# Optimization experiments

Hardware: AMD Instinct MI355X
Metric: run time of the kernel (lower is better)

The kernel has to match this reference:

```python
import jax, jax.numpy as jnp
import numpy as np

EPS = 1e-8  # torch F.cosine_similarity eps


def _l2norm(x):
    # x / max(||x||, eps), matching torch cosine_similarity's clamped denominator
    n = jnp.sqrt(jnp.sum(x * x, axis=-1, keepdims=True))
    return x / jnp.maximum(n, EPS)


def setup_inputs() -> dict:
    key = jax.random.key(0)
    k1, k2, k3 = jax.random.split(key, 3)
    B, S, C, D = 16, 512, 16, 512
    return {
        "output": jax.random.normal(k1, (B, C), dtype=jnp.float32),
        "target_text_feats": jax.random.normal(k2, (B, S, C, D), dtype=jnp.float32),
        "vis_feats": jax.random.normal(k3, (B, S, D), dtype=jnp.float32),
    }


def reference(output, target_text_feats, vis_feats):
    B, S, C, D = target_text_feats.shape
    vn = _l2norm(vis_feats)              # (B, S, D)
    tn = _l2norm(target_text_feats)      # (B, S, C, D)
    # sim[b,p,v,t] = cos(vis[b,v], text[b,t,p]); replaces the per-prompt python loop
    sim = jnp.einsum('bvd,btpd->bpvt', vn, tn)  # (B, C, S, S)
    diag = jnp.diagonal(sim, axis1=-2, axis2=-1)      # (B, C, S): sim[b,p,i,i]
    lse_row = jax.nn.logsumexp(sim, axis=-1)          # CE over text axis (logits_per_image)
    lse_col = jax.nn.logsumexp(sim, axis=-2)          # CE over vis axis  (logits_per_text)
    # per-sample clip loss, averaged over the v axis -> (B, C)
    clip_loss = jnp.mean(0.5 * (lse_row + lse_col) - diag, axis=-1)
    clip_loss = jax.lax.stop_gradient(clip_loss)      # computed under torch.no_grad()

    loss = jnp.mean(jnp.square(output - clip_loss))

    gt_labels = jnp.argmin(clip_loss, axis=-1)        # (B,)
    preds = jnp.argmin(output, axis=-1)               # (B,)
    acc = jnp.mean((preds == gt_labels).astype(jnp.float32)) * 100.0
    prompt_id_preds = jnp.broadcast_to(preds[:, None, None], (B, S, 1))
    return loss, acc, prompt_id_preds
```

## Files before the change

kernel.cpp:

```cpp
#include <hip/hip_runtime.h>

#define EPSN 1e-8f

typedef _Float16 half8 __attribute__((ext_vector_type(8)));
typedef float floatx4 __attribute__((ext_vector_type(4)));

__global__ __launch_bounds__(256) void k_vinv(const float* __restrict__ vis,
                                              float* __restrict__ vinv) {
    int row  = blockIdx.x * 4 + (threadIdx.x >> 6);
    int lane = threadIdx.x & 63;
    const float4* src = reinterpret_cast<const float4*>(vis + (size_t)row * 512);
    float4 a = src[lane];
    float4 b = src[lane + 64];
    float s = a.x*a.x + a.y*a.y + a.z*a.z + a.w*a.w
            + b.x*b.x + b.y*b.y + b.z*b.z + b.w*b.w;
    #pragma unroll
    for (int off = 1; off < 64; off <<= 1) s += __shfl_xor(s, off);
    if (lane == 0) vinv[row] = 1.0f / fmaxf(sqrtf(s), EPSN);
}

#define LDA 40
#define LDB 40

__global__ __launch_bounds__(256, 2) void k_main(
    const float* __restrict__ vis, const float* __restrict__ text,
    const float* __restrict__ vinv,
    float* __restrict__ g_rowsum, float* __restrict__ g_colsum,
    float* __restrict__ g_dsum)
{
    __shared__ _Float16 Ash[256 * LDA];
    __shared__ _Float16 Bsh[128 * LDB];
    __shared__ float tn2[128];
    __shared__ float colS[128];

    const int blk  = blockIdx.x;
    const int vh   = blk & 1;
    const int tb   = (blk >> 1) & 3;
    const int bp   = blk >> 3;
    const int p    = bp & 15;
    const int b    = bp >> 4;
    const int tid  = threadIdx.x;
    const int lane = tid & 63;
    const int wave = tid >> 6;
    const int v0   = vh * 256;
    const int t0   = tb * 128;
    const int m15  = lane & 15;
    const int g4   = lane >> 4;

    if (tid < 128) colS[tid] = 0.f;

    floatx4 acc[4][8];
    floatx4 zf = {0.f, 0.f, 0.f, 0.f};
    #pragma unroll
    for (int mb = 0; mb < 4; ++mb)
        #pragma unroll
        for (int nb = 0; nb < 8; ++nb) acc[mb][nb] = zf;

    const float* visB = vis + (size_t)b * 512 * 512 + (size_t)v0 * 512;
    const int arow = tid >> 2;
    const int ako  = (tid & 3) * 8;
    const int brow0 = tid >> 2;
    const int brow1 = 64 + (tid >> 2);
    const int bko  = (tid & 3) * 8;
    const float* textRow0 =
        text + ((size_t)((b * 512 + t0 + brow0) * 16 + p)) * 512;
    const float* textRow1 =
        text + ((size_t)((b * 512 + t0 + brow1) * 16 + p)) * 512;

    float sq0 = 0.f, sq1 = 0.f;

    for (int kc = 0; kc < 16; ++kc) {
        const int k0 = kc * 32;
        #pragma unroll
        for (int c = 0; c < 4; ++c) {
            int row = c * 64 + arow;
            const float4* s4 =
                reinterpret_cast<const float4*>(visB + (size_t)row * 512 + k0 + ako);
            float4 f0 = s4[0], f1 = s4[1];
            half8 h = { (_Float16)f0.x, (_Float16)f0.y, (_Float16)f0.z, (_Float16)f0.w,
                        (_Float16)f1.x, (_Float16)f1.y, (_Float16)f1.z, (_Float16)f1.w };
            *reinterpret_cast<half8*>(&Ash[row * LDA + ako]) = h;
        }
        {
            const float4* s4 = reinterpret_cast<const float4*>(textRow0 + k0 + bko);
            float4 f0 = s4[0], f1 = s4[1];
            sq0 += f0.x*f0.x + f0.y*f0.y + f0.z*f0.z + f0.w*f0.w
                 + f1.x*f1.x + f1.y*f1.y + f1.z*f1.z + f1.w*f1.w;
            half8 h = { (_Float16)f0.x, (_Float16)f0.y, (_Float16)f0.z, (_Float16)f0.w,
                        (_Float16)f1.x, (_Float16)f1.y, (_Float16)f1.z, (_Float16)f1.w };
            *reinterpret_cast<half8*>(&Bsh[brow0 * LDB + bko]) = h;
        }
        {
            const float4* s4 = reinterpret_cast<const float4*>(textRow1 + k0 + bko);
            float4 f0 = s4[0], f1 = s4[1];
            sq1 += f0.x*f0.x + f0.y*f0.y + f0.z*f0.z + f0.w*f0.w
                 + f1.x*f1.x + f1.y*f1.y + f1.z*f1.z + f1.w*f1.w;
            half8 h = { (_Float16)f0.x, (_Float16)f0.y, (_Float16)f0.z, (_Float16)f0.w,
                        (_Float16)f1.x, (_Float16)f1.y, (_Float16)f1.z, (_Float16)f1.w };
            *reinterpret_cast<half8*>(&Bsh[brow1 * LDB + bko]) = h;
        }
        __syncthreads();
        half8 af[4];
        #pragma unroll
        for (int mb = 0; mb < 4; ++mb)
            af[mb] = *reinterpret_cast<const half8*>(
                &Ash[(wave * 64 + mb * 16 + m15) * LDA + g4 * 8]);
        #pragma unroll
        for (int nb = 0; nb < 8; ++nb) {
            half8 bf = *reinterpret_cast<const half8*>(
                &Bsh[(nb * 16 + m15) * LDB + g4 * 8]);
            #pragma unroll
            for (int mb = 0; mb < 4; ++mb)
                acc[mb][nb] = __builtin_amdgcn_mfma_f32_16x16x32_f16(
                    af[mb], bf, acc[mb][nb], 0, 0, 0);
        }
        __syncthreads();
    }

    sq0 += __shfl_xor(sq0, 1); sq0 += __shfl_xor(sq0, 2);
    sq1 += __shfl_xor(sq1, 1); sq1 += __shfl_xor(sq1, 2);
    if ((tid & 3) == 0) {
        tn2[brow0] = 1.0f / fmaxf(sqrtf(sq0), EPSN);
        tn2[brow1] = 1.0f / fmaxf(sqrtf(sq1), EPSN);
    }
    __syncthreads();

    float tinvc[8];
    #pragma unroll
    for (int nb = 0; nb < 8; ++nb) tinvc[nb] = tn2[nb * 16 + m15];

    float colpart[8];
    #pragma unroll
    for (int nb = 0; nb < 8; ++nb) colpart[nb] = 0.f;
    float dsum = 0.f;

    #pragma unroll
    for (int mb = 0; mb < 4; ++mb) {
        #pragma unroll
        for (int r = 0; r < 4; ++r) {
            int vglob = v0 + wave * 64 + mb * 16 + g4 * 4 + r;
            float vi  = vinv[b * 512 + vglob];
            float rp  = 0.f;
            #pragma unroll
            for (int nb = 0; nb < 8; ++nb) {
                float sim  = acc[mb][nb][r] * vi * tinvc[nb];
                int tglob  = t0 + nb * 16 + m15;
                if (vglob == tglob) dsum += sim;
                float e = __expf(sim);
                rp += e;
                colpart[nb] += e;
            }
            rp += __shfl_xor(rp, 1);
            rp += __shfl_xor(rp, 2);
            rp += __shfl_xor(rp, 4);
            rp += __shfl_xor(rp, 8);
            if (m15 == 0)
                atomicAdd(&g_rowsum[(size_t)bp * 512 + vglob], rp);
        }
    }
    #pragma unroll
    for (int nb = 0; nb < 8; ++nb) {
        float cp = colpart[nb];
        cp += __shfl_xor(cp, 16);
        cp += __shfl_xor(cp, 32);
        if (lane < 16) atomicAdd(&colS[nb * 16 + lane], cp);
    }
    #pragma unroll
    for (int off = 1; off < 64; off <<= 1) dsum += __shfl_xor(dsum, off);
    if (lane == 0) atomicAdd(&g_dsum[bp], dsum);
    __syncthreads();
    if (tid < 128)
        atomicAdd(&g_colsum[(size_t)bp * 512 + t0 + tid], colS[tid]);
}

__global__ __launch_bounds__(256) void k_clip(
    const float* __restrict__ g_rowsum, const float* __restrict__ g_colsum,
    const float* __restrict__ g_dsum, float* __restrict__ clip)
{
    __shared__ float red[4];
    int bp = blockIdx.x, tid = threadIdx.x;
    int lane = tid & 63, wave = tid >> 6;
    float s = 0.f;
    #pragma unroll
    for (int c = 0; c < 2; ++c) {
        int i = c * 256 + tid;
        s += 0.5f * (logf(g_rowsum[(size_t)bp * 512 + i]) +
                     logf(g_colsum[(size_t)bp * 512 + i]));
    }
    #pragma unroll
    for (int off = 1; off < 64; off <<= 1) s += __shfl_xor(s, off);
    if (lane == 0) red[wave] = s;
    __syncthreads();
    if (tid == 0)
        clip[bp] = (red[0] + red[1] + red[2] + red[3] - g_dsum[bp]) * (1.0f / 512.0f);
}

__global__ __launch_bounds__(256) void k_final(
    const float* __restrict__ clip, const float* __restrict__ output,
    float* __restrict__ out)
{
    __shared__ float cl[256], ou[256], red[4];
    __shared__ int preds[16];
    int tid = threadIdx.x, lane = tid & 63, wave = tid >> 6;
    cl[tid] = clip[tid];
    ou[tid] = output[tid];
    __syncthreads();
    float d = ou[tid] - cl[tid];
    float s = d * d;
    #pragma unroll
    for (int off = 1; off < 64; off <<= 1) s += __shfl_xor(s, off);
    if (lane == 0) red[wave] = s;
    if (tid < 16) {
        float m = ou[tid * 16]; int a = 0;
        for (int q = 1; q < 16; ++q)
            if (ou[tid * 16 + q] < m) { m = ou[tid * 16 + q]; a = q; }
        preds[tid] = a;
    }
    __syncthreads();
    if (tid == 0) {
        int cnt = 0;
        for (int bb = 0; bb < 16; ++bb) {
            float m = cl[bb * 16]; int a = 0;
            for (int q = 1; q < 16; ++q)
                if (cl[bb * 16 + q] < m) { m = cl[bb * 16 + q]; a = q; }
            cnt += (preds[bb] == a);
        }
        out[0] = (red[0] + red[1] + red[2] + red[3]) * (1.0f / 256.0f);
        out[1] = (float)cnt * (100.0f / 16.0f);
    }
    __syncthreads();
    for (int j = tid; j < 16 * 512; j += 256)
        out[2 + j] = (float)preds[j >> 9];
}

extern "C" void kernel_launch(void* const* d_in, const int* in_sizes, int n_in,
                              void* d_out, int out_size, void* d_ws, size_t ws_size,
                              hipStream_t stream)
{
    const float* output = (const float*)d_in[0];
    const float* text   = (const float*)d_in[1];
    const float* vis    = (const float*)d_in[2];

    float* g_rowsum = (float*)d_ws;
    float* g_colsum = g_rowsum + 256 * 512;
    float* g_dsum   = g_colsum + 256 * 512;
    float* clip     = g_dsum + 256;
    float* vinv     = clip + 256;
    hipMemsetAsync(d_ws, 0, (size_t)(2 * 256 * 512 + 256) * sizeof(float), stream);

    k_vinv <<<2048, 256, 0, stream>>>(vis, vinv);
    k_main <<<2048, 256, 0, stream>>>(vis, text, vinv, g_rowsum, g_colsum, g_dsum);
    k_clip <<<256, 256, 0, stream>>>(g_rowsum, g_colsum, g_dsum, clip);
    k_final<<<1, 256, 0, stream>>>(clip, output, (float*)d_out);
}
```

Measured before the change: 482.6 us.

## Prefetch next K-chunk into registers, fuse vis norm into main kernel, use packed cvt

Loads for the next K chunk of vis and text are issued into registers before the current chunk's shared-memory store completes, so global latency overlaps with MFMA work. The vis row norms are accumulated inside k_main from the same loaded data, which removes the separate k_vinv launch and its extra pass over vis. Float-to-half conversion switches to the packed round-toward-zero instruction. In exchange, register pressure rises from the 16 extra float4 prefetch registers, the last iteration issues a wasted wrap-around load, and rounding changes slightly from round-to-nearest to round-toward-zero.

Result: no change. 476.1 us (-1.4%).

```diff
diff --git a/kernel.cpp b/kernel.cpp
--- a/kernel.cpp
+++ b/kernel.cpp
@@ -3,34 +3,21 @@
 #define EPSN 1e-8f
 
 typedef _Float16 half8 __attribute__((ext_vector_type(8)));
+typedef __fp16 fp16x2 __attribute__((ext_vector_type(2)));
 typedef float floatx4 __attribute__((ext_vector_type(4)));
-
-__global__ __launch_bounds__(256) void k_vinv(const float* __restrict__ vis,
-                                              float* __restrict__ vinv) {
-    int row  = blockIdx.x * 4 + (threadIdx.x >> 6);
-    int lane = threadIdx.x & 63;
-    const float4* src = reinterpret_cast<const float4*>(vis + (size_t)row * 512);
-    float4 a = src[lane];
-    float4 b = src[lane + 64];
-    float s = a.x*a.x + a.y*a.y + a.z*a.z + a.w*a.w
-            + b.x*b.x + b.y*b.y + b.z*b.z + b.w*b.w;
-    #pragma unroll
-    for (int off = 1; off < 64; off <<= 1) s += __shfl_xor(s, off);
-    if (lane == 0) vinv[row] = 1.0f / fmaxf(sqrtf(s), EPSN);
-}
 
 #define LDA 40
 #define LDB 40
 
 __global__ __launch_bounds__(256, 2) void k_main(
     const float* __restrict__ vis, const float* __restrict__ text,
-    const float* __restrict__ vinv,
     float* __restrict__ g_rowsum, float* __restrict__ g_colsum,
     float* __restrict__ g_dsum)
 {
     __shared__ _Float16 Ash[256 * LDA];
     __shared__ _Float16 Bsh[128 * LDB];
     __shared__ float tn2[128];
+    __shared__ float vinvS[256];
     __shared__ float colS[128];
 
     const int blk  = blockIdx.x;
@@ -59,45 +46,67 @@
     const float* visB = vis + (size_t)b * 512 * 512 + (size_t)v0 * 512;
     const int arow = tid >> 2;
     const int ako  = (tid & 3) * 8;
-    const int brow0 = tid >> 2;
-    const int brow1 = 64 + (tid >> 2);
-    const int bko  = (tid & 3) * 8;
-    const float* textRow0 =
-        text + ((size_t)((b * 512 + t0 + brow0) * 16 + p)) * 512;
-    const float* textRow1 =
-        text + ((size_t)((b * 512 + t0 + brow1) * 16 + p)) * 512;
-
+    const float* aBase = visB + (size_t)arow * 512 + ako;
+    const float* tPtr0 =
+        text + ((size_t)((b * 512 + t0 + (tid >> 2)) * 16 + p)) * 512 + (tid & 3) * 8;
+    const float* tPtr1 = tPtr0 + (size_t)64 * 16 * 512;
+
+    float vsq[4] = {0.f, 0.f, 0.f, 0.f};
     float sq0 = 0.f, sq1 = 0.f;
 
+    float4 abuf[4][2];
+    #pragma unroll
+    for (int c = 0; c < 4; ++c) {
+        abuf[c][0] = *reinterpret_cast<const float4*>(aBase + c * 64 * 512);
+        abuf[c][1] = *reinterpret_cast<const float4*>(aBase + c * 64 * 512 + 4);
+    }
+    float4 bbuf[2][2];
+    bbuf[0][0] = *reinterpret_cast<const float4*>(tPtr0);
+    bbuf[0][1] = *reinterpret_cast<const float4*>(tPtr0 + 4);
+    bbuf[1][0] = *reinterpret_cast<const float4*>(tPtr1);
+    bbuf[1][1] = *reinterpret_cast<const float4*>(tPtr1 + 4);
+
     for (int kc = 0; kc < 16; ++kc) {
-        const int k0 = kc * 32;
+        const int kn = ((kc + 1) & 15) * 32;
         #pragma unroll
         for (int c = 0; c < 4; ++c) {
-            int row = c * 64 + arow;
-            const float4* s4 =
-                reinterpret_cast<const float4*>(visB + (size_t)row * 512 + k0 + ako);
-            float4 f0 = s4[0], f1 = s4[1];
-            half8 h = { (_Float16)f0.x, (_Float16)f0.y, (_Float16)f0.z, (_Float16)f0.w,
-                        (_Float16)f1.x, (_Float16)f1.y, (_Float16)f1.z, (_Float16)f1.w };
-            *reinterpret_cast<half8*>(&Ash[row * LDA + ako]) = h;
+            float4 f0 = abuf[c][0], f1 = abuf[c][1];
+            vsq[c] += f0.x*f0.x + f0.y*f0.y + f0.z*f0.z + f0.w*f0.w
+                    + f1.x*f1.x + f1.y*f1.y + f1.z*f1.z + f1.w*f1.w;
+            union { half8 v; fp16x2 p[4]; } u;
+            u.p[0] = __builtin_amdgcn_cvt_pkrtz(f0.x, f0.y);
+            u.p[1] = __builtin_amdgcn_cvt_pkrtz(f0.z, f0.w);
+            u.p[2] = __builtin_amdgcn_cvt_pkrtz(f1.x, f1.y);
+            u.p[3] = __builtin_amdgcn_cvt_pkrtz(f1.z, f1.w);
+            *reinterpret_cast<half8*>(&Ash[(c * 64 + arow) * LDA + ako]) = u.v;
+            abuf[c][0] = *reinterpret_cast<const float4*>(aBase + c * 64 * 512 + kn);
+            abuf[c][1] = *reinterpret_cast<const float4*>(aBase + c * 64 * 512 + kn + 4);
         }
         {
-            const float4* s4 = reinterpret_cast<const float4*>(textRow0 + k0 + bko);
-            float4 f0 = s4[0], f1 = s4[1];
+            float4 f0 = bbuf[0][0], f1 = bbuf[0][1];
             sq0 += f0.x*f0.x + f0.y*f0.y + f0.z*f0.z + f0.w*f0.w
                  + f1.x*f1.x + f1.y*f1.y + f1.z*f1.z + f1.w*f1.w;
-            half8 h = { (_Float16)f0.x, (_Float16)f0.y, (_Float16)f0.z, (_Float16)f0.w,
-                        (_Float16)f1.x, (_Float16)f1.y, (_Float16)f1.z, (_Float16)f1.w };
-            *reinterpret_cast<half8*>(&Bsh[brow0 * LDB + bko]) = h;
+            union { half8 v; fp16x2 p[4]; } u;
+            u.p[0] = __builtin_amdgcn_cvt_pkrtz(f0.x, f0.y);
+            u.p[1] = __builtin_amdgcn_cvt_pkrtz(f0.z, f0.w);
+            u.p[2] = __builtin_amdgcn_cvt_pkrtz(f1.x, f1.y);
+            u.p[3] = __builtin_amdgcn_cvt_pkrtz(f1.z, f1.w);
+            *reinterpret_cast<half8*>(&Bsh[(tid >> 2) * LDB + (tid & 3) * 8]) = u.v;
+            bbuf[0][0] = *reinterpret_cast<const float4*>(tPtr0 + kn);
+            bbuf[0][1] = *reinterpret_cast<const float4*>(tPtr0 + kn + 4);
         }
         {
-            const float4* s4 = reinterpret_cast<const float4*>(textRow1 + k0 + bko);
-            float4 f0 = s4[0], f1 = s4[1];
+            float4 f0 = bbuf[1][0], f1 = bbuf[1][1];
             sq1 += f0.x*f0.x + f0.y*f0.y + f0.z*f0.z + f0.w*f0.w
                  + f1.x*f1.x + f1.y*f1.y + f1.z*f1.z + f1.w*f1.w;
-            half8 h = { (_Float16)f0.x, (_Float16)f0.y, (_Float16)f0.z, (_Float16)f0.w,
-                        (_Float16)f1.x, (_Float16)f1.y, (_Float16)f1.z, (_Float16)f1.w };
-            *reinterpret_cast<half8*>(&Bsh[brow1 * LDB + bko]) = h;
+            union { half8 v; fp16x2 p[4]; } u;
+            u.p[0] = __builtin_amdgcn_cvt_pkrtz(f0.x, f0.y);
+            u.p[1] = __builtin_amdgcn_cvt_pkrtz(f0.z, f0.w);
+            u.p[2] = __builtin_amdgcn_cvt_pkrtz(f1.x, f1.y);
+            u.p[3] = __builtin_amdgcn_cvt_pkrtz(f1.z, f1.w);
+            *reinterpret_cast<half8*>(&Bsh[(64 + (tid >> 2)) * LDB + (tid & 3) * 8]) = u.v;
+            bbuf[1][0] = *reinterpret_cast<const float4*>(tPtr1 + kn);
+            bbuf[1][1] = *reinterpret_cast<const float4*>(tPtr1 + kn + 4);
         }
         __syncthreads();
         half8 af[4];
@@ -117,11 +126,18 @@
         __syncthreads();
     }
 
+    #pragma unroll
+    for (int c = 0; c < 4; ++c) {
+        float s = vsq[c];
+        s += __shfl_xor(s, 1); s += __shfl_xor(s, 2);
+        if ((lane & 3) == 0)
+            vinvS[c * 64 + arow] = 1.0f / fmaxf(sqrtf(s), EPSN);
+    }
     sq0 += __shfl_xor(sq0, 1); sq0 += __shfl_xor(sq0, 2);
     sq1 += __shfl_xor(sq1, 1); sq1 += __shfl_xor(sq1, 2);
     if ((tid & 3) == 0) {
-        tn2[brow0] = 1.0f / fmaxf(sqrtf(sq0), EPSN);
-        tn2[brow1] = 1.0f / fmaxf(sqrtf(sq1), EPSN);
+        tn2[tid >> 2] = 1.0f / fmaxf(sqrtf(sq0), EPSN);
+        tn2[64 + (tid >> 2)] = 1.0f / fmaxf(sqrtf(sq1), EPSN);
     }
     __syncthreads();
 
@@ -138,8 +154,9 @@
     for (int mb = 0; mb < 4; ++mb) {
         #pragma unroll
         for (int r = 0; r < 4; ++r) {
-            int vglob = v0 + wave * 64 + mb * 16 + g4 * 4 + r;
-            float vi  = vinv[b * 512 + vglob];
+            int vloc  = wave * 64 + mb * 16 + g4 * 4 + r;
+            int vglob = v0 + vloc;
+            float vi  = vinvS[vloc];
             float rp  = 0.f;
             #pragma unroll
             for (int nb = 0; nb < 8; ++nb) {
@@ -245,11 +262,9 @@
     float* g_colsum = g_rowsum + 256 * 512;
     float* g_dsum   = g_colsum + 256 * 512;
     float* clip     = g_dsum + 256;
-    float* vinv     = clip + 256;
-    hipMemsetAsync(d_ws, 0, (size_t)(2 * 256 * 512 + 256) * sizeof(float), stream);
-
-    k_vinv <<<2048, 256, 0, stream>>>(vis, vinv);
-    k_main <<<2048, 256, 0, stream>>>(vis, text, vinv, g_rowsum, g_colsum, g_dsum);
+    (void)hipMemsetAsync(d_ws, 0, (size_t)(2 * 256 * 512 + 256) * sizeof(float), stream);
+
+    k_main <<<2048, 256, 0, stream>>>(vis, text, g_rowsum, g_colsum, g_dsum);
     k_clip <<<256, 256, 0, stream>>>(g_rowsum, g_colsum, g_dsum, clip);
     k_final<<<1, 256, 0, stream>>>(clip, output, (float*)d_out);
 }
```

## Use 128x128 tiles with 2x2 wave layout and fuse vis-norm into main kernel

Applied to the files above, without the earlier changes.

Changes the GEMM tile from 256x128 to 128x128 per block, with a 2x2 wave arrangement and 4096 blocks at occupancy hint 4. The vis row norms are now computed inside the main kernel instead of a separate k_vinv launch. Row sums are accumulated in shared memory before one global atomic per row, and fp32-to-fp16 conversion uses packed cvt_pkrtz. The smaller tile reloads the vis and text operands more often (text reads double), which may raise memory traffic on an already bandwidth-heavy kernel; pkrtz rounds toward zero rather than to nearest.

Result: slower. 494.7 us (+2.5%).

```diff
diff --git a/kernel.cpp b/kernel.cpp
--- a/kernel.cpp
+++ b/kernel.cpp
@@ -3,112 +3,110 @@
 #define EPSN 1e-8f
 
 typedef _Float16 half8 __attribute__((ext_vector_type(8)));
+typedef __fp16 fp16x2 __attribute__((ext_vector_type(2)));
 typedef float floatx4 __attribute__((ext_vector_type(4)));
 
-__global__ __launch_bounds__(256) void k_vinv(const float* __restrict__ vis,
-                                              float* __restrict__ vinv) {
-    int row  = blockIdx.x * 4 + (threadIdx.x >> 6);
-    int lane = threadIdx.x & 63;
-    const float4* src = reinterpret_cast<const float4*>(vis + (size_t)row * 512);
-    float4 a = src[lane];
-    float4 b = src[lane + 64];
-    float s = a.x*a.x + a.y*a.y + a.z*a.z + a.w*a.w
-            + b.x*b.x + b.y*b.y + b.z*b.z + b.w*b.w;
-    #pragma unroll
-    for (int off = 1; off < 64; off <<= 1) s += __shfl_xor(s, off);
-    if (lane == 0) vinv[row] = 1.0f / fmaxf(sqrtf(s), EPSN);
-}
-
 #define LDA 40
-#define LDB 40
-
-__global__ __launch_bounds__(256, 2) void k_main(
+
+__global__ __launch_bounds__(256, 4) void k_main(
     const float* __restrict__ vis, const float* __restrict__ text,
-    const float* __restrict__ vinv,
     float* __restrict__ g_rowsum, float* __restrict__ g_colsum,
     float* __restrict__ g_dsum)
 {
-    __shared__ _Float16 Ash[256 * LDA];
-    __shared__ _Float16 Bsh[128 * LDB];
+    __shared__ _Float16 Ash[128 * LDA];
+    __shared__ _Float16 Bsh[128 * LDA];
     __shared__ float tn2[128];
+    __shared__ float vinvS[128];
+    __shared__ float rowS[128];
     __shared__ float colS[128];
 
     const int blk  = blockIdx.x;
-    const int vh   = blk & 1;
-    const int tb   = (blk >> 1) & 3;
-    const int bp   = blk >> 3;
+    const int vq   = blk & 3;
+    const int tb   = (blk >> 2) & 3;
+    const int bp   = blk >> 4;
     const int p    = bp & 15;
     const int b    = bp >> 4;
     const int tid  = threadIdx.x;
     const int lane = tid & 63;
     const int wave = tid >> 6;
-    const int v0   = vh * 256;
-    const int t0   = tb * 128;
+    const int wy   = wave >> 1;
+    const int wx   = wave & 1;
     const int m15  = lane & 15;
     const int g4   = lane >> 4;
 
-    if (tid < 128) colS[tid] = 0.f;
-
-    floatx4 acc[4][8];
+    if (tid < 128) { rowS[tid] = 0.f; colS[tid] = 0.f; }
+
+    floatx4 acc[4][4];
     floatx4 zf = {0.f, 0.f, 0.f, 0.f};
     #pragma unroll
     for (int mb = 0; mb < 4; ++mb)
         #pragma unroll
-        for (int nb = 0; nb < 8; ++nb) acc[mb][nb] = zf;
-
-    const float* visB = vis + (size_t)b * 512 * 512 + (size_t)v0 * 512;
-    const int arow = tid >> 2;
-    const int ako  = (tid & 3) * 8;
-    const int brow0 = tid >> 2;
-    const int brow1 = 64 + (tid >> 2);
-    const int bko  = (tid & 3) * 8;
-    const float* textRow0 =
-        text + ((size_t)((b * 512 + t0 + brow0) * 16 + p)) * 512;
-    const float* textRow1 =
-        text + ((size_t)((b * 512 + t0 + brow1) * 16 + p)) * 512;
-
-    float sq0 = 0.f, sq1 = 0.f;
+        for (int nb = 0; nb < 4; ++nb) acc[mb][nb] = zf;
+
+    const int srow = tid >> 1;
+    const int sko  = (tid & 1) * 16;
+    const float* aPtr =
+        vis + (size_t)b * 512 * 512 + (size_t)(vq * 128 + srow) * 512 + sko;
+    const float* bPtr =
+        text + ((size_t)((b * 512 + tb * 128 + srow) * 16 + p)) * 512 + sko;
+
+    float vsq = 0.f, tsq = 0.f;
 
     for (int kc = 0; kc < 16; ++kc) {
-        const int k0 = kc * 32;
-        #pragma unroll
-        for (int c = 0; c < 4; ++c) {
-            int row = c * 64 + arow;
-            const float4* s4 =
-                reinterpret_cast<const float4*>(visB + (size_t)row * 512 + k0 + ako);
-            float4 f0 = s4[0], f1 = s4[1];
-            half8 h = { (_Float16)f0.x, (_Float16)f0.y, (_Float16)f0.z, (_Float16)f0.w,
-                        (_Float16)f1.x, (_Float16)f1.y, (_Float16)f1.z, (_Float16)f1.w };
-            *reinterpret_cast<half8*>(&Ash[row * LDA + ako]) = h;
-        }
+        float4 a0 = *reinterpret_cast<const float4*>(aPtr);
+        float4 a1 = *reinterpret_cast<const float4*>(aPtr + 4);
+        float4 a2 = *reinterpret_cast<const float4*>(aPtr + 8);
+        float4 a3 = *reinterpret_cast<const float4*>(aPtr + 12);
+        float4 b0 = *reinterpret_cast<const float4*>(bPtr);
+        float4 b1 = *reinterpret_cast<const float4*>(bPtr + 4);
+        float4 b2 = *reinterpret_cast<const float4*>(bPtr + 8);
+        float4 b3 = *reinterpret_cast<const float4*>(bPtr + 12);
+        aPtr += 32; bPtr += 32;
+
+        vsq += a0.x*a0.x + a0.y*a0.y + a0.z*a0.z + a0.w*a0.w
+             + a1.x*a1.x + a1.y*a1.y + a1.z*a1.z + a1.w*a1.w
+             + a2.x*a2.x + a2.y*a2.y + a2.z*a2.z + a2.w*a2.w
+             + a3.x*a3.x + a3.y*a3.y + a3.z*a3.z + a3.w*a3.w;
         {
-            const float4* s4 = reinterpret_cast<const float4*>(textRow0 + k0 + bko);
-            float4 f0 = s4[0], f1 = s4[1];
-            sq0 += f0.x*f0.x + f0.y*f0.y + f0.z*f0.z + f0.w*f0.w
-                 + f1.x*f1.x + f1.y*f1.y + f1.z*f1.z + f1.w*f1.w;
-            half8 h = { (_Float16)f0.x, (_Float16)f0.y, (_Float16)f0.z, (_Float16)f0.w,
-                        (_Float16)f1.x, (_Float16)f1.y, (_Float16)f1.z, (_Float16)f1.w };
-            *reinterpret_cast<half8*>(&Bsh[brow0 * LDB + bko]) = h;
-        }
+            union { half8 v; fp16x2 q[4]; } u;
+            u.q[0] = __builtin_amdgcn_cvt_pkrtz(a0.x, a0.y);
+            u.q[1] = __builtin_amdgcn_cvt_pkrtz(a0.z, a0.w);
+            u.q[2] = __builtin_amdgcn_cvt_pkrtz(a1.x, a1.y);
+            u.q[3] = __builtin_amdgcn_cvt_pkrtz(a1.z, a1.w);
+            *reinterpret_cast<half8*>(&Ash[srow * LDA + sko]) = u.v;
+            u.q[0] = __builtin_amdgcn_cvt_pkrtz(a2.x, a2.y);
+            u.q[1] = __builtin_amdgcn_cvt_pkrtz(a2.z, a2.w);
+            u.q[2] = __builtin_amdgcn_cvt_pkrtz(a3.x, a3.y);
+            u.q[3] = __builtin_amdgcn_cvt_pkrtz(a3.z, a3.w);
+            *reinterpret_cast<half8*>(&Ash[srow * LDA + sko + 8]) = u.v;
+        }
+        tsq += b0.x*b0.x + b0.y*b0.y + b0.z*b0.z + b0.w*b0.w
+             + b1.x*b1.x + b1.y*b1.y + b1.z*b1.z + b1.w*b1.w
+             + b2.x*b2.x + b2.y*b2.y + b2.z*b2.z + b2.w*b2.w
+             + b3.x*b3.x + b3.y*b3.y + b3.z*b3.z + b3.w*b3.w;
         {
-            const float4* s4 = reinterpret_cast<const float4*>(textRow1 + k0 + bko);
-            float4 f0 = s4[0], f1 = s4[1];
-            sq1 += f0.x*f0.x + f0.y*f0.y + f0.z*f0.z + f0.w*f0.w
-                 + f1.x*f1.x + f1.y*f1.y + f1.z*f1.z + f1.w*f1.w;
-            half8 h = { (_Float16)f0.x, (_Float16)f0.y, (_Float16)f0.z, (_Float16)f0.w,
-                        (_Float16)f1.x, (_Float16)f1.y, (_Float16)f1.z, (_Float16)f1.w };
-            *reinterpret_cast<half8*>(&Bsh[brow1 * LDB + bko]) = h;
+            union { half8 v; fp16x2 q[4]; } u;
+            u.q[0] = __builtin_amdgcn_cvt_pkrtz(b0.x, b0.y);
+            u.q[1] = __builtin_amdgcn_cvt_pkrtz(b0.z, b0.w);
+            u.q[2] = __builtin_amdgcn_cvt_pkrtz(b1.x, b1.y);
+            u.q[3] = __builtin_amdgcn_cvt_pkrtz(b1.z, b1.w);
+            *reinterpret_cast<half8*>(&Bsh[srow * LDA + sko]) = u.v;
+            u.q[0] = __builtin_amdgcn_cvt_pkrtz(b2.x, b2.y);
+            u.q[1] = __builtin_amdgcn_cvt_pkrtz(b2.z, b2.w);
+            u.q[2] = __builtin_amdgcn_cvt_pkrtz(b3.x, b3.y);
+            u.q[3] = __builtin_amdgcn_cvt_pkrtz(b3.z, b3.w);
+            *reinterpret_cast<half8*>(&Bsh[srow * LDA + sko + 8]) = u.v;
         }
         __syncthreads();
         half8 af[4];
         #pragma unroll
         for (int mb = 0; mb < 4; ++mb)
             af[mb] = *reinterpret_cast<const half8*>(
-                &Ash[(wave * 64 + mb * 16 + m15) * LDA + g4 * 8]);
-        #pragma unroll
-        for (int nb = 0; nb < 8; ++nb) {
+                &Ash[(wy * 64 + mb * 16 + m15) * LDA + g4 * 8]);
+        #pragma unroll
+        for (int nb = 0; nb < 4; ++nb) {
             half8 bf = *reinterpret_cast<const half8*>(
-                &Bsh[(nb * 16 + m15) * LDB + g4 * 8]);
+                &Bsh[(wx * 64 + nb * 16 + m15) * LDA + g4 * 8]);
             #pragma unroll
             for (int mb = 0; mb < 4; ++mb)
                 acc[mb][nb] = __builtin_amdgcn_mfma_f32_16x16x32_f16(
@@ -117,34 +115,35 @@
         __syncthreads();
     }
 
-    sq0 += __shfl_xor(sq0, 1); sq0 += __shfl_xor(sq0, 2);
-    sq1 += __shfl_xor(sq1, 1); sq1 += __shfl_xor(sq1, 2);
-    if ((tid & 3) == 0) {
-        tn2[brow0] = 1.0f / fmaxf(sqrtf(sq0), EPSN);
-        tn2[brow1] = 1.0f / fmaxf(sqrtf(sq1), EPSN);
-    }
-    __syncthreads();
-
-    float tinvc[8];
-    #pragma unroll
-    for (int nb = 0; nb < 8; ++nb) tinvc[nb] = tn2[nb * 16 + m15];
-
-    float colpart[8];
-    #pragma unroll
-    for (int nb = 0; nb < 8; ++nb) colpart[nb] = 0.f;
+    vsq += __shfl_xor(vsq, 1);
+    tsq += __shfl_xor(tsq, 1);
+    if ((tid & 1) == 0) {
+        vinvS[srow] = 1.0f / fmaxf(sqrtf(vsq), EPSN);
+        tn2[srow]   = 1.0f / fmaxf(sqrtf(tsq), EPSN);
+    }
+    __syncthreads();
+
+    float tinvc[4];
+    #pragma unroll
+    for (int nb = 0; nb < 4; ++nb) tinvc[nb] = tn2[wx * 64 + nb * 16 + m15];
+
+    float colpart[4];
+    #pragma unroll
+    for (int nb = 0; nb < 4; ++nb) colpart[nb] = 0.f;
     float dsum = 0.f;
 
     #pragma unroll
     for (int mb = 0; mb < 4; ++mb) {
         #pragma unroll
         for (int r = 0; r < 4; ++r) {
-            int vglob = v0 + wave * 64 + mb * 16 + g4 * 4 + r;
-            float vi  = vinv[b * 512 + vglob];
+            int vloc  = wy * 64 + mb * 16 + g4 * 4 + r;
+            int vglob = vq * 128 + vloc;
+            float vi  = vinvS[vloc];
             float rp  = 0.f;
             #pragma unroll
-            for (int nb = 0; nb < 8; ++nb) {
+            for (int nb = 0; nb < 4; ++nb) {
                 float sim  = acc[mb][nb][r] * vi * tinvc[nb];
-                int tglob  = t0 + nb * 16 + m15;
+                int tglob  = tb * 128 + wx * 64 + nb * 16 + m15;
                 if (vglob == tglob) dsum += sim;
                 float e = __expf(sim);
                 rp += e;
@@ -154,23 +153,26 @@
             rp += __shfl_xor(rp, 2);
             rp += __shfl_xor(rp, 4);
             rp += __shfl_xor(rp, 8);
-            if (m15 == 0)
-                atomicAdd(&g_rowsum[(size_t)bp * 512 + vglob], rp);
-        }
-    }
-    #pragma unroll
-    for (int nb = 0; nb < 8; ++nb) {
+            if (m15 == 0) atomicAdd(&rowS[vloc], rp);
+        }
+    }
+    #pragma unroll
+    for (int nb = 0; nb < 4; ++nb) {
         float cp = colpart[nb];
         cp += __shfl_xor(cp, 16);
         cp += __shfl_xor(cp, 32);
-        if (lane < 16) atomicAdd(&colS[nb * 16 + lane], cp);
-    }
-    #pragma unroll
-    for (int off = 1; off < 64; off <<= 1) dsum += __shfl_xor(dsum, off);
-    if (lane == 0) atomicAdd(&g_dsum[bp], dsum);
-    __syncthreads();
-    if (tid < 128)
-        atomicAdd(&g_colsum[(size_t)bp * 512 + t0 + tid], colS[tid]);
+        if (lane < 16) atomicAdd(&colS[wx * 64 + nb * 16 + lane], cp);
+    }
+    if (vq == tb) {
+        #pragma unroll
+        for (int off = 1; off < 64; off <<= 1) dsum += __shfl_xor(dsum, off);
+        if (lane == 0) atomicAdd(&g_dsum[bp], dsum);
+    }
+    __syncthreads();
+    if (tid < 128) {
+        atomicAdd(&g_rowsum[(size_t)bp * 512 + vq * 128 + tid], rowS[tid]);
+        atomicAdd(&g_colsum[(size_t)bp * 512 + tb * 128 + tid], colS[tid]);
+    }
 }
 
 __global__ __launch_bounds__(256) void k_clip(
@@ -245,11 +247,9 @@
     float* g_colsum = g_rowsum + 256 * 512;
     float* g_dsum   = g_colsum + 256 * 512;
     float* clip     = g_dsum + 256;
-    float* vinv     = clip + 256;
-    hipMemsetAsync(d_ws, 0, (size_t)(2 * 256 * 512 + 256) * sizeof(float), stream);
-
-    k_vinv <<<2048, 256, 0, stream>>>(vis, vinv);
-    k_main <<<2048, 256, 0, stream>>>(vis, text, vinv, g_rowsum, g_colsum, g_dsum);
+    (void)hipMemsetAsync(d_ws, 0, (size_t)(2 * 256 * 512 + 256) * sizeof(float), stream);
+
+    k_main <<<4096, 256, 0, stream>>>(vis, text, g_rowsum, g_colsum, g_dsum);
     k_clip <<<256, 256, 0, stream>>>(g_rowsum, g_colsum, g_dsum, clip);
     k_final<<<1, 256, 0, stream>>>(clip, output, (float*)d_out);
 }
```
